# Kernel optimization log

Hardware: AMD Instinct MI355X
Metric: run time of the kernel (lower is better)

Reference implementation:

```python
import jax, jax.numpy as jnp
import numpy as np

M, K = 4096, 4096
ORDER = 12  # ceil(log2(max(M,K)))
BATCH, SEQ = 4, 2048


def _hilbert_d_grid(order, m, k):
    """Vectorized xy->d Hilbert-curve index for an m x k grid (numpy, int)."""
    n = 1 << order
    ii, jj = np.meshgrid(np.arange(m, dtype=np.int64), np.arange(k, dtype=np.int64), indexing='ij')
    x, y = jj.copy(), ii.copy()
    d = np.zeros_like(x)
    s = n >> 1
    while s > 0:
        rx = ((x & s) > 0).astype(np.int64)
        ry = ((y & s) > 0).astype(np.int64)
        d += s * s * ((3 * rx) ^ ry)
        # rotate quadrant
        swap = ry == 0
        flip = swap & (rx == 1)
        xf = np.where(flip, s - 1 - x, x)
        yf = np.where(flip, s - 1 - y, y)
        x = np.where(swap, yf, xf)
        y = np.where(swap, xf, yf)
        s >>= 1
    return d.astype(np.int32)


def setup_inputs() -> dict:
    key = jax.random.key(0)
    k1, = jax.random.split(key, 1)
    x = jax.random.normal(k1, (BATCH, SEQ, K), dtype=jnp.float32)
    # dna init per __init__: [4.0,1.0,1.0,0.5,0.5,0.5] with dna[0] += (seed%100)/10 for seed=42
    dna = jnp.array([8.2, 1.0, 1.0, 0.5, 0.5, 0.5], dtype=jnp.float32)
    bias = jnp.zeros((M,), dtype=jnp.float32)
    hilbert_d = jnp.asarray(_hilbert_d_grid(ORDER, M, K))  # [M, K] int32
    return {"x": x, "dna": dna, "bias": bias, "hilbert_d": hilbert_d}


def reference(x, dna, bias, hilbert_d):
    # dna is detached in the torch forward (weights built from numpy copy)
    p = jax.lax.stop_gradient(dna)
    m_p, a, b, n1, n2, n3 = p[0], p[1], p[2], p[3], p[4], p[5]
    total = jnp.float32((1 << ORDER) * (1 << ORDER))
    theta = hilbert_d.astype(jnp.float32) * (2.0 * jnp.pi / total)  # [M,K]
    ang = m_p * theta * 0.25
    base = jnp.abs(jnp.cos(ang) / a) ** n2 + jnp.abs(jnp.sin(ang) / b) ** n3
    r = base ** (-1.0 / n1)  # Gielis superformula radius, [M,K]
    w = (r - r.mean()) / (jnp.std(r, ddof=1) + 1e-9)  # torch .std() is unbiased
    scale = jnp.float32(1.0 / np.sqrt(K))
    return jnp.einsum('bsk,mk->bsm', x, w) * scale + bias
```

## Files before the change

kernel.cpp:

```cpp
#include <hip/hip_runtime.h>

#define M_DIM 4096
#define K_DIM 4096
#define NR_DIM 8192
#define TOTAL_ELEMS (M_DIM * K_DIM)

typedef unsigned short u16;
typedef unsigned int u32;
typedef __bf16 bf16x8 __attribute__((ext_vector_type(8)));
typedef float f32x4 __attribute__((ext_vector_type(4)));
typedef u16 u16x8 __attribute__((ext_vector_type(8)));

__device__ __forceinline__ u16 f2b(float f) {
    u32 v;
    __builtin_memcpy(&v, &f, sizeof(v));
    v += 0x7FFFu + ((v >> 16) & 1u);
    return (u16)(v >> 16);
}

__device__ __forceinline__ void abs_sincos(float ang, float* s, float* c) {
    float q = rintf(ang * 0.636619772f);
    float r1 = fmaf(q, -1.57079637e+00f, ang);
    float r = fmaf(q, 4.37113883e-08f, r1);
    float r2 = r * r;
    float ts = fmaf(r2, -1.9840874e-04f, 8.3333310e-03f);
    ts = fmaf(r2, ts, -1.6666667e-01f);
    float sp = fmaf(r * r2, ts, r);
    float tc = fmaf(r2, -1.3888378e-03f, 4.1666638e-02f);
    tc = fmaf(r2, tc, -5.0e-01f);
    float cp = fmaf(r2, tc, 1.0f);
    bool sw = (((int)q) & 1) != 0;
    *s = sw ? cp : sp;
    *c = sw ? sp : cp;
}

__device__ __forceinline__ float compute_r_fast(int d, float c_ang) {
    float s, c;
    abs_sincos((float)d * c_ang, &s, &c);
    float base = __builtin_amdgcn_sqrtf(fabsf(c)) + __builtin_amdgcn_sqrtf(fabsf(s));
    return __builtin_amdgcn_rcpf(base * base);
}

__device__ __noinline__ float compute_r_gen(int d, float c_ang, float inv_a,
                                            float inv_b, float n2, float n3, float e) {
    float s, c;
    abs_sincos((float)d * c_ang, &s, &c);
    float ca = fabsf(c) * fabsf(inv_a);
    float sb = fabsf(s) * fabsf(inv_b);
    float t1 = (n2 == 0.5f) ? sqrtf(ca) : ((n2 == 1.0f) ? ca : powf(ca, n2));
    float t2 = (n3 == 0.5f) ? sqrtf(sb) : ((n3 == 1.0f) ? sb : powf(sb, n3));
    float base = t1 + t2;
    if (e == -2.0f) { float ib = __builtin_amdgcn_rcpf(base); return ib * ib; }
    if (e == -1.0f) return __builtin_amdgcn_rcpf(base);
    return powf(base, e);
}

__device__ __forceinline__ bool dna_is_fast(const float* p) {
    return (p[1] == 1.0f) & (p[2] == 1.0f) & (p[3] == 0.5f) &
           (p[4] == 0.5f) & (p[5] == 0.5f);
}

__global__ void __launch_bounds__(256) reduce_kernel(const float* __restrict__ dna,
                                                     double* __restrict__ sums) {
    float p[6];
#pragma unroll
    for (int i = 0; i < 6; i++) p[i] = dna[i];
    float c_ang = (float)((double)p[0] * 6.283185307179586 / 67108864.0);

    double s = 0.0, s2 = 0.0;
    int idx = blockIdx.x * blockDim.x + threadIdx.x;
    int stride = gridDim.x * blockDim.x;
    if (dna_is_fast(p)) {
        for (int d = idx; d < TOTAL_ELEMS; d += stride) {
            float r = compute_r_fast(d, c_ang);
            s += (double)r;
            s2 += (double)r * (double)r;
        }
    } else {
        float inv_a = 1.0f / p[1], inv_b = 1.0f / p[2], e = -1.0f / p[3];
        for (int d = idx; d < TOTAL_ELEMS; d += stride) {
            float r = compute_r_gen(d, c_ang, inv_a, inv_b, p[4], p[5], e);
            s += (double)r;
            s2 += (double)r * (double)r;
        }
    }
#pragma unroll
    for (int off = 32; off > 0; off >>= 1) {
        s += __shfl_down(s, off);
        s2 += __shfl_down(s2, off);
    }
    __shared__ double ls[4], ls2[4];
    int lane = threadIdx.x & 63, w = threadIdx.x >> 6;
    if (lane == 0) { ls[w] = s; ls2[w] = s2; }
    __syncthreads();
    if (threadIdx.x == 0) {
        atomicAdd(&sums[0], ls[0] + ls[1] + ls[2] + ls[3]);
        atomicAdd(&sums[1], ls2[0] + ls2[1] + ls2[2] + ls2[3]);
    }
}

__global__ void __launch_bounds__(256) build_w_kernel(const int* __restrict__ hd,
                                                      const float* __restrict__ dna,
                                                      const double* __restrict__ sums,
                                                      u16* __restrict__ W) {
    float p[6];
#pragma unroll
    for (int i = 0; i < 6; i++) p[i] = dna[i];
    float c_ang = (float)((double)p[0] * 6.283185307179586 / 67108864.0);

    const double cnt = (double)TOTAL_ELEMS;
    double sum = sums[0], sumsq = sums[1];
    float meanf = (float)(sum / cnt);
    float stdf = (float)sqrt((sumsq - sum * sum / cnt) / (cnt - 1.0));
    float sc = 0.015625f / (stdf + 1e-9f);

    int idx = blockIdx.x * blockDim.x + threadIdx.x;
    int stride = gridDim.x * blockDim.x;
    if (dna_is_fast(p)) {
        for (int i = idx * 4; i < TOTAL_ELEMS; i += stride * 4) {
            int4 d4 = *(const int4*)(hd + i);
            ushort4 o;
            o.x = f2b((compute_r_fast(d4.x, c_ang) - meanf) * sc);
            o.y = f2b((compute_r_fast(d4.y, c_ang) - meanf) * sc);
            o.z = f2b((compute_r_fast(d4.z, c_ang) - meanf) * sc);
            o.w = f2b((compute_r_fast(d4.w, c_ang) - meanf) * sc);
            *(ushort4*)(W + i) = o;
        }
    } else {
        float inv_a = 1.0f / p[1], inv_b = 1.0f / p[2], e = -1.0f / p[3];
        for (int i = idx * 4; i < TOTAL_ELEMS; i += stride * 4) {
            int4 d4 = *(const int4*)(hd + i);
            ushort4 o;
            o.x = f2b((compute_r_gen(d4.x, c_ang, inv_a, inv_b, p[4], p[5], e) - meanf) * sc);
            o.y = f2b((compute_r_gen(d4.y, c_ang, inv_a, inv_b, p[4], p[5], e) - meanf) * sc);
            o.z = f2b((compute_r_gen(d4.z, c_ang, inv_a, inv_b, p[4], p[5], e) - meanf) * sc);
            o.w = f2b((compute_r_gen(d4.w, c_ang, inv_a, inv_b, p[4], p[5], e) - meanf) * sc);
            *(ushort4*)(W + i) = o;
        }
    }
}

__global__ void __launch_bounds__(256) convert_x_kernel(const float* __restrict__ x,
                                                        u16* __restrict__ xb) {
    int i = (blockIdx.x * blockDim.x + threadIdx.x) * 8;
    const float4* xv = (const float4*)(x + i);
    float4 a = xv[0], b = xv[1];
    u16x8 o;
    o[0] = f2b(a.x); o[1] = f2b(a.y); o[2] = f2b(a.z); o[3] = f2b(a.w);
    o[4] = f2b(b.x); o[5] = f2b(b.y); o[6] = f2b(b.z); o[7] = f2b(b.w);
    *(u16x8*)(xb + i) = o;
}

#define BM 256
#define BN 256
#define BK 64

__device__ __forceinline__ void gld_lds16(const u16* g, u16* l) {
    __builtin_amdgcn_global_load_lds(
        (const __attribute__((address_space(1))) void*)g,
        (__attribute__((address_space(3))) void*)l,
        16, 0, 0);
}

#define FENCE asm volatile("" ::: "memory")
#define WAIT_LGKM0 asm volatile("s_waitcnt lgkmcnt(0)" ::: "memory")
#define WAIT_VM6 asm volatile("s_waitcnt vmcnt(6)" ::: "memory")
#define WAIT_VM8 asm volatile("s_waitcnt vmcnt(8)" ::: "memory")

#define LOAD_AF(h, bufv, ks)                                                  \
    _Pragma("unroll") for (int m = 0; m < 4; ++m) {                           \
        int row = wr * 128 + ((h) * 4 + m) * 16 + lrow;                       \
        af[m] = *(const bf16x8*)(&sA[bufv][ks][row * 32 + oA]);               \
    }

#define LOAD_BF(bufv, ks)                                                     \
    _Pragma("unroll") for (int n = 0; n < 4; ++n) {                           \
        int row = wc * 64 + n * 16 + lrow;                                    \
        bfr[n] = *(const bf16x8*)(&sB[bufv][ks][row * 32 + oA]);              \
    }

#define MFMA_HALF(h)                                                          \
    __builtin_amdgcn_s_setprio(1);                                            \
    _Pragma("unroll") for (int m = 0; m < 4; ++m)                             \
        _Pragma("unroll") for (int n = 0; n < 4; ++n)                         \
            acc[(h) * 4 + m][n] = __builtin_amdgcn_mfma_f32_16x16x32_bf16(    \
                af[m], bfr[n], acc[(h) * 4 + m][n], 0, 0, 0);                 \
    __builtin_amdgcn_s_setprio(0)

__global__ void __launch_bounds__(512, 2) gemm_kernel(const u16* __restrict__ A,
                                                      const u16* __restrict__ B,
                                                      const float* __restrict__ bias,
                                                      float* __restrict__ C) {
    __shared__ __align__(16) u16 sA[2][2][BM * 32];
    __shared__ __align__(16) u16 sB[2][2][BN * 32];

    const int tid = threadIdx.x;
    const int lane = tid & 63;
    const int wave = tid >> 6;
    const int wr = wave >> 2;
    const int wc = wave & 3;
    const int lrow = lane & 15;
    const int lq = lane >> 4;
    const int oA = ((lq ^ ((lrow >> 1) & 3)) << 3);

    const int flat = blockIdx.y * 16 + blockIdx.x;
    const int swz = (flat & 7) * 64 + (flat >> 3);
    const int bx = swz & 15;
    const int by = swz >> 4;
    const int i0 = by * BM;
    const int j0 = bx * BN;

    const int srow0 = tid >> 2;
    const int olog = (tid & 3) ^ ((srow0 >> 1) & 3);
    const int aoff0 = (i0 + srow0) * K_DIM + olog * 8;
    const int aoff1 = aoff0 + 128 * K_DIM;
    const int boff0 = (j0 + srow0) * K_DIM + olog * 8;
    const int boff1 = boff0 + 128 * K_DIM;
    const int lds_l0 = tid * 8;
    const int lds_l1 = (tid + 512) * 8;

    auto stage = [&](const u16* base, int off0, int off1, u16* slot, int kb) {
        gld_lds16(base + off0 + kb, slot + lds_l0);
        gld_lds16(base + off1 + kb, slot + lds_l1);
    };

    const f32x4 vzero = {0.f, 0.f, 0.f, 0.f};
    f32x4 acc[8][4];
#pragma unroll
    for (int a = 0; a < 8; a++)
#pragma unroll
        for (int b = 0; b < 4; b++) acc[a][b] = vzero;

    stage(A, aoff0, aoff1, sA[0][0], 0);
    stage(B, boff0, boff1, sB[0][0], 0);
    stage(A, aoff0, aoff1, sA[0][1], 32);
    stage(B, boff0, boff1, sB[0][1], 32);
    stage(A, aoff0, aoff1, sA[1][0], 64);
    stage(B, boff0, boff1, sB[1][0], 64);
    WAIT_VM8;
    FENCE;
    __builtin_amdgcn_s_barrier();

    for (int kt = 0; kt < K_DIM / BK; ++kt) {
        const int bufv = kt & 1;
        const int kb1 = (kt + 1 < 64 ? kt + 1 : 63) * 64 + 32;
        const int kb2 = (kt + 2 < 64 ? kt + 2 : 63) * 64;
        bf16x8 af[4], bfr[4];

        LOAD_AF(0, bufv, 0);
        LOAD_BF(bufv, 0);
        stage(A, aoff0, aoff1, sA[bufv ^ 1][1], kb1);
        FENCE;
        __builtin_amdgcn_s_barrier();
        WAIT_LGKM0;
        MFMA_HALF(0);
        FENCE;
        __builtin_amdgcn_s_barrier();

        LOAD_AF(1, bufv, 0);
        stage(B, boff0, boff1, sB[bufv ^ 1][1], kb1);
        FENCE;
        __builtin_amdgcn_s_barrier();
        WAIT_LGKM0;
        MFMA_HALF(1);
        WAIT_VM6;
        FENCE;
        __builtin_amdgcn_s_barrier();

        LOAD_AF(0, bufv, 1);
        LOAD_BF(bufv, 1);
        stage(A, aoff0, aoff1, sA[bufv][0], kb2);
        FENCE;
        __builtin_amdgcn_s_barrier();
        WAIT_LGKM0;
        MFMA_HALF(0);
        FENCE;
        __builtin_amdgcn_s_barrier();

        LOAD_AF(1, bufv, 1);
        stage(B, boff0, boff1, sB[bufv][0], kb2);
        FENCE;
        __builtin_amdgcn_s_barrier();
        WAIT_LGKM0;
        MFMA_HALF(1);
        WAIT_VM6;
        FENCE;
        __builtin_amdgcn_s_barrier();
    }

#pragma unroll
    for (int ni = 0; ni < 4; ++ni) {
        long j = j0 + wc * 64 + ni * 16 + lrow;
        float bv = bias[j];
#pragma unroll
        for (int mi = 0; mi < 8; ++mi) {
            long ib = i0 + wr * 128 + mi * 16 + lq * 4;
#pragma unroll
            for (int r = 0; r < 4; ++r) {
                C[(ib + r) * M_DIM + j] = acc[mi][ni][r] + bv;
            }
        }
    }
}

extern "C" void kernel_launch(void* const* d_in, const int* in_sizes, int n_in,
                              void* d_out, int out_size, void* d_ws, size_t ws_size,
                              hipStream_t stream) {
    const float* x = (const float*)d_in[0];
    const float* dna = (const float*)d_in[1];
    const float* bias = (const float*)d_in[2];
    const int* hd = (const int*)d_in[3];
    float* out = (float*)d_out;

    double* sums = (double*)d_ws;
    u16* W = (u16*)((char*)d_ws + 256);
    u16* Xb = (u16*)((char*)d_ws + 256 + (size_t)TOTAL_ELEMS * 2);

    hipMemsetAsync(d_ws, 0, 256, stream);
    reduce_kernel<<<dim3(1024), dim3(256), 0, stream>>>(dna, sums);
    build_w_kernel<<<dim3(2048), dim3(256), 0, stream>>>(hd, dna, sums, W);
    convert_x_kernel<<<dim3((NR_DIM * K_DIM) / (256 * 8)), dim3(256), 0, stream>>>(x, Xb);
    gemm_kernel<<<dim3(M_DIM / BN, NR_DIM / BM), dim3(512), 0, stream>>>(Xb, W, bias, out);
}
```

Before: 593.4 us.

## Double-buffer A fragments to prefetch LDS reads ahead of MFMA phases

Splits the A-fragment registers into two sets so the next half-tile's LDS reads are issued before the current MFMA block runs. The explicit lgkmcnt(0) waits are removed, leaving the compiler to insert waits only where a fragment is actually used. The first A fragment is loaded before the loop, and the prologue vmcnt wait is tightened so the extra staged data has landed. This adds register pressure and relies on the existing barrier placement to keep LDS reads of the next buffer ordered after its async writes.

```diff
diff --git a/kernel.cpp b/kernel.cpp
--- a/kernel.cpp
+++ b/kernel.cpp
@@ -163,28 +163,26 @@
 }
 
 #define FENCE asm volatile("" ::: "memory")
-#define WAIT_LGKM0 asm volatile("s_waitcnt lgkmcnt(0)" ::: "memory")
 #define WAIT_VM6 asm volatile("s_waitcnt vmcnt(6)" ::: "memory")
-#define WAIT_VM8 asm volatile("s_waitcnt vmcnt(8)" ::: "memory")
-
-#define LOAD_AF(h, bufv, ks)                                                  \
+
+#define ISSUE_AF(dst, bufv, ks, h)                                            \
     _Pragma("unroll") for (int m = 0; m < 4; ++m) {                           \
         int row = wr * 128 + ((h) * 4 + m) * 16 + lrow;                       \
-        af[m] = *(const bf16x8*)(&sA[bufv][ks][row * 32 + oA]);               \
-    }
-
-#define LOAD_BF(bufv, ks)                                                     \
+        dst[m] = *(const bf16x8*)(&sA[bufv][ks][row * 32 + oA]);              \
+    }
+
+#define ISSUE_BF(dst, bufv, ks)                                               \
     _Pragma("unroll") for (int n = 0; n < 4; ++n) {                           \
         int row = wc * 64 + n * 16 + lrow;                                    \
-        bfr[n] = *(const bf16x8*)(&sB[bufv][ks][row * 32 + oA]);              \
-    }
-
-#define MFMA_HALF(h)                                                          \
+        dst[n] = *(const bf16x8*)(&sB[bufv][ks][row * 32 + oA]);              \
+    }
+
+#define MFMA_HALF(h, afb, bfb)                                                \
     __builtin_amdgcn_s_setprio(1);                                            \
     _Pragma("unroll") for (int m = 0; m < 4; ++m)                             \
         _Pragma("unroll") for (int n = 0; n < 4; ++n)                         \
             acc[(h) * 4 + m][n] = __builtin_amdgcn_mfma_f32_16x16x32_bf16(    \
-                af[m], bfr[n], acc[(h) * 4 + m][n], 0, 0, 0);                 \
+                afb[m], bfb[n], acc[(h) * 4 + m][n], 0, 0, 0);                \
     __builtin_amdgcn_s_setprio(0)
 
 __global__ void __launch_bounds__(512, 2) gemm_kernel(const u16* __restrict__ A,
@@ -237,52 +235,51 @@
     stage(B, boff0, boff1, sB[0][1], 32);
     stage(A, aoff0, aoff1, sA[1][0], 64);
     stage(B, boff0, boff1, sB[1][0], 64);
-    WAIT_VM8;
+    WAIT_VM6;
     FENCE;
     __builtin_amdgcn_s_barrier();
+
+    bf16x8 af_a[4], af_b[4], bfr[4];
+    ISSUE_AF(af_a, 0, 0, 0);
+    FENCE;
 
     for (int kt = 0; kt < K_DIM / BK; ++kt) {
         const int bufv = kt & 1;
         const int kb1 = (kt + 1 < 64 ? kt + 1 : 63) * 64 + 32;
         const int kb2 = (kt + 2 < 64 ? kt + 2 : 63) * 64;
-        bf16x8 af[4], bfr[4];
-
-        LOAD_AF(0, bufv, 0);
-        LOAD_BF(bufv, 0);
+
+        ISSUE_BF(bfr, bufv, 0);
+        ISSUE_AF(af_b, bufv, 0, 1);
         stage(A, aoff0, aoff1, sA[bufv ^ 1][1], kb1);
         FENCE;
         __builtin_amdgcn_s_barrier();
-        WAIT_LGKM0;
-        MFMA_HALF(0);
-        FENCE;
-        __builtin_amdgcn_s_barrier();
-
-        LOAD_AF(1, bufv, 0);
+        MFMA_HALF(0, af_a, bfr);
+        FENCE;
+        __builtin_amdgcn_s_barrier();
+
+        ISSUE_AF(af_a, bufv, 1, 0);
         stage(B, boff0, boff1, sB[bufv ^ 1][1], kb1);
         FENCE;
         __builtin_amdgcn_s_barrier();
-        WAIT_LGKM0;
-        MFMA_HALF(1);
+        MFMA_HALF(1, af_b, bfr);
         WAIT_VM6;
         FENCE;
         __builtin_amdgcn_s_barrier();
 
-        LOAD_AF(0, bufv, 1);
-        LOAD_BF(bufv, 1);
+        ISSUE_BF(bfr, bufv, 1);
+        ISSUE_AF(af_b, bufv, 1, 1);
         stage(A, aoff0, aoff1, sA[bufv][0], kb2);
         FENCE;
         __builtin_amdgcn_s_barrier();
-        WAIT_LGKM0;
-        MFMA_HALF(0);
-        FENCE;
-        __builtin_amdgcn_s_barrier();
-
-        LOAD_AF(1, bufv, 1);
+        MFMA_HALF(0, af_a, bfr);
+        FENCE;
+        __builtin_amdgcn_s_barrier();
+
+        ISSUE_AF(af_a, bufv ^ 1, 0, 0);
         stage(B, boff0, boff1, sB[bufv][0], kb2);
         FENCE;
         __builtin_amdgcn_s_barrier();
-        WAIT_LGKM0;
-        MFMA_HALF(1);
+        MFMA_HALF(1, af_b, bfr);
         WAIT_VM6;
         FENCE;
         __builtin_amdgcn_s_barrier();
```

After: 610.7 us. 1.03x slower.
